# Kernel optimization log

Hardware: AMD Instinct MI355X
Metric: run time of the kernel (lower is better)

The kernel has to match this reference:

```python
import jax, jax.numpy as jnp
import numpy as np

B, t, FEAT, N, E = 128, 16, 256, 1024, 8192


def setup_inputs() -> dict:
    key = jax.random.key(0)
    k = jax.random.split(key, 9)
    s = 1.0 / np.sqrt(FEAT).astype(np.float32)
    x = jax.random.normal(k[0], (B, t, FEAT), jnp.float32)
    nodes = jax.random.normal(k[1], (B, N, FEAT), jnp.float32)
    edges = jax.random.randint(k[2], (B, 2, E), 0, 256).astype(jnp.int32)
    weights = jax.random.uniform(k[3], (B, 1, E), jnp.float32)
    T = jax.random.randint(k[4], (B,), 0, N - t).astype(jnp.int32)
    taus = jnp.full((B,), t, dtype=jnp.int32)  # no ragged padding: taus == t
    W_self1 = jax.random.normal(k[5], (FEAT, FEAT), jnp.float32) * s
    W_msg1 = jax.random.normal(k[6], (FEAT, FEAT), jnp.float32) * s
    W_self2 = jax.random.normal(k[7], (FEAT, FEAT), jnp.float32) * s
    W_msg2 = jax.random.normal(k[8], (FEAT, FEAT), jnp.float32) * s
    return dict(x=x, taus=taus, nodes=nodes, edges=edges, weights=weights, T=T,
                W_self1=W_self1, W_msg1=W_msg1, W_self2=W_self2, W_msg2=W_msg2)


def _gcm(x, nodes, weights, edges, T, Ws1, Wm1, Ws2, Wm2):
    Bn, tn, feat = x.shape
    Nn = nodes.shape[1]
    # --- scatter new nodes into the fixed-size node buffer ---
    b_idx = jnp.repeat(jnp.arange(Bn), tn)                       # [B*t]
    tau_idx = (T[:, None] + jnp.arange(tn)).reshape(-1)          # [B*t]
    nodes = nodes.at[b_idx, tau_idx].set(x.reshape(Bn * tn, feat))
    # --- to_batch: flatten ragged per-batch graphs into one big graph ---
    flat = nodes.reshape(Bn * Nn, feat)                          # [B*N, feat]
    off = (jnp.arange(Bn) * Nn)[:, None]                         # per-batch node offset
    valid = (edges[:, 0] >= 0) & (edges[:, 1] >= 0)              # -1 marks invalid edges
    src = jnp.where(valid, edges[:, 0] + off, 0).reshape(-1)     # [B*E]
    dst = jnp.where(valid, edges[:, 1] + off, 0).reshape(-1)
    ew = (weights[:, 0] * valid).reshape(-1)                     # invalid edges -> weight 0
    # --- 2-layer edge-weighted GraphConv GNN (tanh activation) ---
    def layer(h, Ws, Wm):
        agg = jax.ops.segment_sum(ew[:, None] * h[src], dst, num_segments=Bn * Nn)
        return jnp.tanh(h @ Ws + agg @ Wm)
    h = layer(flat, Ws1, Wm1)
    h = layer(h, Ws2, Wm2)
    # --- gather GNN outputs for the newly inserted nodes ---
    out_idx = b_idx * Nn + tau_idx
    mx = h[out_idx].reshape(Bn, tn, feat)
    return mx, nodes


def reference(x, taus, nodes, edges, weights, T, W_self1, W_msg1, W_self2, W_msg2):
    mx, new_nodes = _gcm(x, nodes, weights, edges, T, W_self1, W_msg1, W_self2, W_msg2)
    return (mx, new_nodes, edges, weights, T + taus)
```

## Files before the change

### kernel.cpp

```cpp
#include <hip/hip_runtime.h>
#include <math.h>

#define BB    128
#define TTW   16
#define FEATN 256
#define NNODE 1024
#define NEDGE 8192
#define MROW  272
#define M1    (BB*MROW)
#define M2    (BB*TTW)

#define OUT_MX    0
#define OUT_NODES (BB*TTW*FEATN)
#define OUT_EDGES (OUT_NODES + BB*NNODE*FEATN)
#define OUT_W     (OUT_EDGES + BB*2*NEDGE)
#define OUT_TT    (OUT_W + BB*NEDGE)

typedef short bf16x8 __attribute__((ext_vector_type(8)));
typedef float f32x4  __attribute__((ext_vector_type(4)));

__device__ inline unsigned short f2bf(float f) {
    unsigned int u = __float_as_uint(f);
    return (unsigned short)((u + 0x7fffu + ((u >> 16) & 1u)) >> 16);
}
__device__ inline float tanh_fast(float x) {
    return 1.f - 2.f / (__expf(2.f * x) + 1.f);
}

__global__ void k_pass(const float4* __restrict__ nodes4, const float4* __restrict__ x4,
                       const int* __restrict__ T, float4* __restrict__ out4) {
    int idx = blockIdx.x * 256 + threadIdx.x;
    int b   = idx >> 16;
    int row = (idx >> 6) & 1023;
    int f   = idx & 63;
    int dT  = row - T[b];
    const float4* src = ((unsigned)dT < 16u) ? (x4 + ((size_t)b * 16 + dT) * 64 + f)
                                             : (nodes4 + idx);
    out4[idx] = *src;
}

__global__ void k_misc(const int4* __restrict__ e4, const float4* __restrict__ w4,
                       const int* __restrict__ T, const int* __restrict__ taus,
                       float* __restrict__ out) {
    int i = blockIdx.x * 256 + threadIdx.x;
    if (i < 524288) {
        int4 e = e4[i];
        float4 o = make_float4((float)e.x, (float)e.y, (float)e.z, (float)e.w);
        ((float4*)(out + OUT_EDGES))[i] = o;
    } else if (i < 786432) {
        ((float4*)(out + OUT_W))[i - 524288] = w4[i - 524288];
    } else if (i < 786560) {
        int b = i - 786432;
        out[OUT_TT + b] = (float)(T[b] + taus[b]);
    }
}

__global__ void k_wconv(const float* __restrict__ Ws1, const float* __restrict__ Wm1,
                        const float* __restrict__ Ws2, const float* __restrict__ Wm2,
                        unsigned short* __restrict__ Wt1, unsigned short* __restrict__ Wt2) {
    int i = blockIdx.x * 256 + threadIdx.x;
    int layer = i >> 17;
    int j = i & 131071;
    int k = j >> 8, n = j & 255;
    const float* Ws = layer ? Ws2 : Ws1;
    const float* Wm = layer ? Wm2 : Wm1;
    float v = (k < 256) ? Ws[(size_t)k * 256 + n] : Wm[(size_t)(k - 256) * 256 + n];
    unsigned short* Wt = layer ? Wt2 : Wt1;
    Wt[(size_t)n * 512 + k] = f2bf(v);
}

__global__ void k_prep_x(const float* __restrict__ nodes, const float* __restrict__ x,
                         const int* __restrict__ T, unsigned short* __restrict__ Xc1) {
    int idx = blockIdx.x * 256 + threadIdx.x;
    int g  = idx >> 5;
    int c8 = idx & 31;
    int b = g / MROW, r = g % MROW;
    int Tb = T[b];
    const float* src;
    if (r >= 256)                       src = x + ((size_t)b * 16 + (r - 256)) * 256;
    else if ((unsigned)(r - Tb) < 16u)  src = x + ((size_t)b * 16 + (r - Tb)) * 256;
    else                                src = nodes + ((size_t)b * 1024 + r) * 256;
    float4 v0 = *(const float4*)(src + c8 * 8);
    float4 v1 = *(const float4*)(src + c8 * 8 + 4);
    uint4 p;
    p.x = f2bf(v0.x) | ((unsigned)f2bf(v0.y) << 16);
    p.y = f2bf(v0.z) | ((unsigned)f2bf(v0.w) << 16);
    p.z = f2bf(v1.x) | ((unsigned)f2bf(v1.y) << 16);
    p.w = f2bf(v1.z) | ((unsigned)f2bf(v1.w) << 16);
    *(uint4*)(Xc1 + (size_t)g * 512 + c8 * 8) = p;
}

__global__ void k_bucket(const int* __restrict__ edges, const float* __restrict__ w,
                         int2* __restrict__ sw, int* __restrict__ bstart) {
    int b = blockIdx.x, tid = threadIdx.x;
    __shared__ int cnt[256];
    __shared__ int pos[256];
    cnt[tid] = 0;
    __syncthreads();
    const int* src = edges + (size_t)b * 2 * NEDGE;
    const int* dst = src + NEDGE;
    for (int e = tid; e < NEDGE; e += 256) atomicAdd(&cnt[dst[e]], 1);
    __syncthreads();
    int my = cnt[tid], v = my;
    for (int off = 1; off < 256; off <<= 1) {
        int u = 0;
        if (tid >= off) u = cnt[tid - off];
        __syncthreads();
        cnt[tid] = v = v + u;
        __syncthreads();
    }
    int start = v - my;
    bstart[b * 264 + tid] = start;
    if (tid == 0) bstart[b * 264 + 256] = NEDGE;
    pos[tid] = start;
    __syncthreads();
    const float* wb = w + (size_t)b * NEDGE;
    for (int e = tid; e < NEDGE; e += 256) {
        int d = dst[e];
        int p = atomicAdd(&pos[d], 1);
        sw[(size_t)b * NEDGE + p] = make_int2(src[e], __float_as_int(wb[e]));
    }
}

__global__ void k_agg1(const int2* __restrict__ sw, const int* __restrict__ bstart,
                       const int* __restrict__ T, unsigned short* __restrict__ Xc1) {
    int wid  = blockIdx.x * 4 + (threadIdx.x >> 6);
    int lane = threadIdx.x & 63;
    int b = wid / MROW, r = wid % MROW;
    int d = (r < 256) ? r : (T[b] + (r - 256));
    float4 acc = make_float4(0.f, 0.f, 0.f, 0.f);
    if (d < 256) {
        int e0 = bstart[b * 264 + d];
        int e1 = bstart[b * 264 + d + 1];
        const int2* swb = sw + (size_t)b * NEDGE;
        const unsigned short* Xb = Xc1 + (size_t)b * MROW * 512;
        for (int e = e0; e < e1; ++e) {
            int2 p = swb[e];
            float wt = __int_as_float(p.y);
            uint2 q = *((const uint2*)(Xb + (size_t)p.x * 512) + lane);
            acc.x = fmaf(wt, __uint_as_float(q.x << 16),          acc.x);
            acc.y = fmaf(wt, __uint_as_float(q.x & 0xffff0000u),  acc.y);
            acc.z = fmaf(wt, __uint_as_float(q.y << 16),          acc.z);
            acc.w = fmaf(wt, __uint_as_float(q.y & 0xffff0000u),  acc.w);
        }
    }
    uint2 o;
    o.x = f2bf(acc.x) | ((unsigned)f2bf(acc.y) << 16);
    o.y = f2bf(acc.z) | ((unsigned)f2bf(acc.w) << 16);
    *(uint2*)(Xc1 + (size_t)wid * 512 + 256 + lane * 4) = o;
}

template <int OBF16>
__global__ __launch_bounds__(256, 2) void k_gemm(const unsigned short* __restrict__ Xc,
                                                 const unsigned short* __restrict__ Wt,
                                                 void* __restrict__ outp) {
    int tile_m = blockIdx.x >> 1;
    int tile_n = blockIdx.x & 1;
    int tid  = threadIdx.x;
    int wv   = tid >> 6, lane = tid & 63;
    int wm   = wv >> 1, wn = wv & 1;
    int lm   = lane & 15, lq = lane >> 4;

    __shared__ short As[128 * 32];
    __shared__ short Bs[128 * 32];

    f32x4 acc[4][4];
#pragma unroll
    for (int mi = 0; mi < 4; ++mi)
#pragma unroll
        for (int ni = 0; ni < 4; ++ni) acc[mi][ni] = (f32x4){0.f, 0.f, 0.f, 0.f};

    for (int kc = 0; kc < 16; ++kc) {
        if (kc) __syncthreads();
#pragma unroll
        for (int p = 0; p < 2; ++p) {
            int slot = p * 256 + tid;
            int row = slot >> 2, seg = slot & 3;
            ((uint4*)As)[slot] = *(const uint4*)(Xc + ((size_t)(tile_m * 128 + row)) * 512 + kc * 32 + seg * 8);
            ((uint4*)Bs)[slot] = *(const uint4*)(Wt + ((size_t)(tile_n * 128 + row)) * 512 + kc * 32 + seg * 8);
        }
        __syncthreads();

        bf16x8 af[4], bfr[4];
#pragma unroll
        for (int mi = 0; mi < 4; ++mi)
            af[mi] = ((const bf16x8*)As)[(wm * 64 + mi * 16 + lm) * 4 + lq];
#pragma unroll
        for (int ni = 0; ni < 4; ++ni)
            bfr[ni] = ((const bf16x8*)Bs)[(wn * 64 + ni * 16 + lm) * 4 + lq];
#pragma unroll
        for (int mi = 0; mi < 4; ++mi)
#pragma unroll
            for (int ni = 0; ni < 4; ++ni)
                acc[mi][ni] = __builtin_amdgcn_mfma_f32_16x16x32_bf16(af[mi], bfr[ni], acc[mi][ni], 0, 0, 0);
    }

#pragma unroll
    for (int mi = 0; mi < 4; ++mi) {
#pragma unroll
        for (int ni = 0; ni < 4; ++ni) {
            int n = tile_n * 128 + wn * 64 + ni * 16 + lm;
#pragma unroll
            for (int r = 0; r < 4; ++r) {
                int m = tile_m * 128 + wm * 64 + mi * 16 + lq * 4 + r;
                float v = tanh_fast(acc[mi][ni][r]);
                if (OBF16) ((unsigned short*)outp)[(size_t)m * 256 + n] = f2bf(v);
                else       ((float*)outp)[(size_t)m * 256 + n] = v;
            }
        }
    }
}

__global__ void k_agg2(const unsigned short* __restrict__ h1, const int2* __restrict__ sw,
                       const int* __restrict__ bstart, const int* __restrict__ T,
                       unsigned short* __restrict__ Xc2) {
    int g2   = blockIdx.x * 4 + (threadIdx.x >> 6);
    int lane = threadIdx.x & 63;
    int b = g2 >> 4, i = g2 & 15;
    ((uint2*)(Xc2 + (size_t)g2 * 512))[lane] =
        ((const uint2*)(h1 + (size_t)(b * MROW + 256 + i) * 256))[lane];
    int d = T[b] + i;
    float4 acc = make_float4(0.f, 0.f, 0.f, 0.f);
    if (d < 256) {
        int e0 = bstart[b * 264 + d];
        int e1 = bstart[b * 264 + d + 1];
        const int2* swb = sw + (size_t)b * NEDGE;
        const unsigned short* hb = h1 + (size_t)b * MROW * 256;
        for (int e = e0; e < e1; ++e) {
            int2 p = swb[e];
            float wt = __int_as_float(p.y);
            uint2 q = *((const uint2*)(hb + (size_t)p.x * 256) + lane);
            acc.x = fmaf(wt, __uint_as_float(q.x << 16),          acc.x);
            acc.y = fmaf(wt, __uint_as_float(q.x & 0xffff0000u),  acc.y);
            acc.z = fmaf(wt, __uint_as_float(q.y << 16),          acc.z);
            acc.w = fmaf(wt, __uint_as_float(q.y & 0xffff0000u),  acc.w);
        }
    }
    uint2 o;
    o.x = f2bf(acc.x) | ((unsigned)f2bf(acc.y) << 16);
    o.y = f2bf(acc.z) | ((unsigned)f2bf(acc.w) << 16);
    *(uint2*)(Xc2 + (size_t)g2 * 512 + 256 + lane * 4) = o;
}

extern "C" void kernel_launch(void* const* d_in, const int* in_sizes, int n_in,
                              void* d_out, int out_size, void* d_ws, size_t ws_size,
                              hipStream_t stream) {
    const float* x       = (const float*)d_in[0];
    const int*   taus    = (const int*)d_in[1];
    const float* nodes   = (const float*)d_in[2];
    const int*   edges   = (const int*)d_in[3];
    const float* weights = (const float*)d_in[4];
    const int*   T       = (const int*)d_in[5];
    const float* Ws1     = (const float*)d_in[6];
    const float* Wm1     = (const float*)d_in[7];
    const float* Ws2     = (const float*)d_in[8];
    const float* Wm2     = (const float*)d_in[9];
    float* out = (float*)d_out;

    char* ws = (char*)d_ws;
    int2*           sw     = (int2*)ws;
    int*            bstart = (int*)(ws + 8388608);
    unsigned short* Xc1    = (unsigned short*)(ws + 8523776);
    unsigned short* h1     = (unsigned short*)(ws + 44175360);
    unsigned short* Xc2    = (unsigned short*)(ws + 62001152);
    unsigned short* Wt1    = (unsigned short*)(ws + 64098304);
    unsigned short* Wt2    = (unsigned short*)(ws + 64360448);

    float* out_nodes = out + OUT_NODES;

    k_pass  <<<32768, 256, 0, stream>>>((const float4*)nodes, (const float4*)x, T, (float4*)out_nodes);
    k_misc  <<<3073, 256, 0, stream>>>((const int4*)edges, (const float4*)weights, T, taus, out);
    k_wconv <<<1024, 256, 0, stream>>>(Ws1, Wm1, Ws2, Wm2, Wt1, Wt2);
    k_prep_x<<<4352, 256, 0, stream>>>(nodes, x, T, Xc1);
    k_bucket<<<BB, 256, 0, stream>>>(edges, weights, sw, bstart);
    k_agg1  <<<8704, 256, 0, stream>>>(sw, bstart, T, Xc1);
    k_gemm<1><<<272 * 2, 256, 0, stream>>>(Xc1, Wt1, h1);
    k_agg2  <<<512, 256, 0, stream>>>(h1, sw, bstart, T, Xc2);
    k_gemm<0><<<16 * 2, 256, 0, stream>>>(Xc2, Wt2, out + OUT_MX);
}
```

Measured before the change: 470.0 us.

## Replace layer-1 sparse gather aggregation with dense adjacency MFMA GEMM

Builds a dense per-batch 256x256 fp32 weighted adjacency matrix using atomic adds, transposes the bf16 node features, and computes the layer-1 aggregation as a batched bf16 MFMA GEMM instead of a per-destination edge gather loop. A small kernel then copies the aggregation rows for the inserted window. This trades irregular gathers for dense matrix work. It adds zeroing and atomic scatter over a 32 MB adjacency buffer, a transpose kernel, and rounds the edge weights to bf16, which can lose precision.

```diff
diff --git a/kernel.cpp b/kernel.cpp
--- a/kernel.cpp
+++ b/kernel.cpp
@@ -8,7 +8,6 @@
 #define NEDGE 8192
 #define MROW  272
 #define M1    (BB*MROW)
-#define M2    (BB*TTW)
 
 #define OUT_MX    0
 #define OUT_NODES (BB*TTW*FEATN)
@@ -90,6 +89,44 @@
     *(uint4*)(Xc1 + (size_t)g * 512 + c8 * 8) = p;
 }
 
+__global__ void k_xt(const unsigned short* __restrict__ Xc1, unsigned short* __restrict__ Xt) {
+    int b  = blockIdx.x >> 4;
+    int tr = (blockIdx.x >> 2) & 3;
+    int tc = blockIdx.x & 3;
+    __shared__ unsigned short S[64][72];
+#pragma unroll
+    for (int p = 0; p < 2; ++p) {
+        int slot = p * 256 + threadIdx.x;
+        int r = slot >> 3, c8 = slot & 7;
+        uint4 v = *(const uint4*)(Xc1 + ((size_t)(b * MROW + tr * 64 + r)) * 512 + tc * 64 + c8 * 8);
+        *(uint4*)&S[r][c8 * 8] = v;
+    }
+    __syncthreads();
+#pragma unroll
+    for (int p = 0; p < 2; ++p) {
+        int slot = p * 256 + threadIdx.x;
+        int r2 = slot >> 3, c8 = slot & 7;
+        unsigned short tmp[8];
+#pragma unroll
+        for (int j = 0; j < 8; ++j) tmp[j] = S[c8 * 8 + j][r2];
+        *(uint4*)(Xt + ((size_t)b << 16) + (size_t)(tc * 64 + r2) * 256 + tr * 64 + c8 * 8) = *(uint4*)tmp;
+    }
+}
+
+__global__ void k_zero(float4* __restrict__ p) {
+    int i = blockIdx.x * 256 + threadIdx.x;
+    p[i] = make_float4(0.f, 0.f, 0.f, 0.f);
+}
+
+__global__ void k_adj(const int* __restrict__ edges, const float* __restrict__ w,
+                      float* __restrict__ W_adj) {
+    int i = blockIdx.x * 256 + threadIdx.x;
+    int b = i >> 13, e = i & 8191;
+    const int* eb = edges + (size_t)b * 2 * NEDGE;
+    int s = eb[e], d = eb[NEDGE + e];
+    atomicAdd(&W_adj[((size_t)b << 16) + (d << 8) + s], w[(size_t)b * NEDGE + e]);
+}
+
 __global__ void k_bucket(const int* __restrict__ edges, const float* __restrict__ w,
                          int2* __restrict__ sw, int* __restrict__ bstart) {
     int b = blockIdx.x, tid = threadIdx.x;
@@ -122,32 +159,88 @@
     }
 }
 
-__global__ void k_agg1(const int2* __restrict__ sw, const int* __restrict__ bstart,
-                       const int* __restrict__ T, unsigned short* __restrict__ Xc1) {
-    int wid  = blockIdx.x * 4 + (threadIdx.x >> 6);
-    int lane = threadIdx.x & 63;
-    int b = wid / MROW, r = wid % MROW;
-    int d = (r < 256) ? r : (T[b] + (r - 256));
-    float4 acc = make_float4(0.f, 0.f, 0.f, 0.f);
-    if (d < 256) {
-        int e0 = bstart[b * 264 + d];
-        int e1 = bstart[b * 264 + d + 1];
-        const int2* swb = sw + (size_t)b * NEDGE;
-        const unsigned short* Xb = Xc1 + (size_t)b * MROW * 512;
-        for (int e = e0; e < e1; ++e) {
-            int2 p = swb[e];
-            float wt = __int_as_float(p.y);
-            uint2 q = *((const uint2*)(Xb + (size_t)p.x * 512) + lane);
-            acc.x = fmaf(wt, __uint_as_float(q.x << 16),          acc.x);
-            acc.y = fmaf(wt, __uint_as_float(q.x & 0xffff0000u),  acc.y);
-            acc.z = fmaf(wt, __uint_as_float(q.y << 16),          acc.z);
-            acc.w = fmaf(wt, __uint_as_float(q.y & 0xffff0000u),  acc.w);
-        }
-    }
-    uint2 o;
-    o.x = f2bf(acc.x) | ((unsigned)f2bf(acc.y) << 16);
-    o.y = f2bf(acc.z) | ((unsigned)f2bf(acc.w) << 16);
-    *(uint2*)(Xc1 + (size_t)wid * 512 + 256 + lane * 4) = o;
+__global__ __launch_bounds__(256, 2) void k_aggemm(const float* __restrict__ W_adj,
+                                                   const unsigned short* __restrict__ Xt,
+                                                   unsigned short* __restrict__ Xc1) {
+    int b = blockIdx.x >> 2;
+    int tile_m = (blockIdx.x >> 1) & 1, tile_n = blockIdx.x & 1;
+    int tid = threadIdx.x;
+    int wv = tid >> 6, lane = tid & 63;
+    int wm = wv >> 1, wn = wv & 1;
+    int lm = lane & 15, lq = lane >> 4;
+
+    __shared__ short As[128 * 32];
+    __shared__ short Bs[128 * 32];
+
+    f32x4 acc[4][4];
+#pragma unroll
+    for (int mi = 0; mi < 4; ++mi)
+#pragma unroll
+        for (int ni = 0; ni < 4; ++ni) acc[mi][ni] = (f32x4){0.f, 0.f, 0.f, 0.f};
+
+    const float* Ab = W_adj + ((size_t)b << 16) + (size_t)tile_m * 128 * 256;
+    const unsigned short* Bb = Xt + ((size_t)b << 16) + (size_t)tile_n * 128 * 256;
+
+    for (int kc = 0; kc < 8; ++kc) {
+        if (kc) __syncthreads();
+#pragma unroll
+        for (int p = 0; p < 4; ++p) {
+            int slot = p * 256 + tid;
+            int row = slot >> 3, seg = slot & 7;
+            float4 v = *(const float4*)(Ab + (size_t)row * 256 + kc * 32 + seg * 4);
+            uint2 pk;
+            pk.x = f2bf(v.x) | ((unsigned)f2bf(v.y) << 16);
+            pk.y = f2bf(v.z) | ((unsigned)f2bf(v.w) << 16);
+            *(uint2*)(As + row * 32 + seg * 4) = pk;
+        }
+#pragma unroll
+        for (int p = 0; p < 2; ++p) {
+            int slot = p * 256 + tid;
+            int row = slot >> 2, seg = slot & 3;
+            ((uint4*)Bs)[slot] = *(const uint4*)(Bb + (size_t)row * 256 + kc * 32 + seg * 8);
+        }
+        __syncthreads();
+
+        bf16x8 af[4], bfr[4];
+#pragma unroll
+        for (int mi = 0; mi < 4; ++mi)
+            af[mi] = ((const bf16x8*)As)[(wm * 64 + mi * 16 + lm) * 4 + lq];
+#pragma unroll
+        for (int ni = 0; ni < 4; ++ni)
+            bfr[ni] = ((const bf16x8*)Bs)[(wn * 64 + ni * 16 + lm) * 4 + lq];
+#pragma unroll
+        for (int mi = 0; mi < 4; ++mi)
+#pragma unroll
+            for (int ni = 0; ni < 4; ++ni)
+                acc[mi][ni] = __builtin_amdgcn_mfma_f32_16x16x32_bf16(af[mi], bfr[ni], acc[mi][ni], 0, 0, 0);
+    }
+
+#pragma unroll
+    for (int mi = 0; mi < 4; ++mi) {
+#pragma unroll
+        for (int ni = 0; ni < 4; ++ni) {
+            int n = tile_n * 128 + wn * 64 + ni * 16 + lm;
+#pragma unroll
+            for (int r = 0; r < 4; ++r) {
+                int m = tile_m * 128 + wm * 64 + mi * 16 + lq * 4 + r;
+                Xc1[((size_t)(b * MROW + m)) * 512 + 256 + n] = f2bf(acc[mi][ni][r]);
+            }
+        }
+    }
+}
+
+__global__ void k_fixwin(const int* __restrict__ T, unsigned short* __restrict__ Xc1) {
+    int b = blockIdx.x;
+    int Tb = T[b];
+#pragma unroll
+    for (int p = 0; p < 2; ++p) {
+        int slot = p * 256 + threadIdx.x;
+        int i = slot >> 5, c = slot & 31;
+        int d = Tb + i;
+        uint4 v = make_uint4(0u, 0u, 0u, 0u);
+        if (d < 256) v = *(const uint4*)(Xc1 + ((size_t)(b * MROW + d)) * 512 + 256 + c * 8);
+        *(uint4*)(Xc1 + ((size_t)(b * MROW + 256 + i)) * 512 + 256 + c * 8) = v;
+    }
 }
 
 template <int OBF16>
@@ -262,19 +355,25 @@
     int*            bstart = (int*)(ws + 8388608);
     unsigned short* Xc1    = (unsigned short*)(ws + 8523776);
     unsigned short* h1     = (unsigned short*)(ws + 44175360);
+    unsigned short* Xt     = (unsigned short*)(ws + 44175360);
     unsigned short* Xc2    = (unsigned short*)(ws + 62001152);
     unsigned short* Wt1    = (unsigned short*)(ws + 64098304);
     unsigned short* Wt2    = (unsigned short*)(ws + 64360448);
+    float*          W_adj  = (float*)(ws + 64622592);
 
     float* out_nodes = out + OUT_NODES;
 
-    k_pass  <<<32768, 256, 0, stream>>>((const float4*)nodes, (const float4*)x, T, (float4*)out_nodes);
-    k_misc  <<<3073, 256, 0, stream>>>((const int4*)edges, (const float4*)weights, T, taus, out);
-    k_wconv <<<1024, 256, 0, stream>>>(Ws1, Wm1, Ws2, Wm2, Wt1, Wt2);
-    k_prep_x<<<4352, 256, 0, stream>>>(nodes, x, T, Xc1);
-    k_bucket<<<BB, 256, 0, stream>>>(edges, weights, sw, bstart);
-    k_agg1  <<<8704, 256, 0, stream>>>(sw, bstart, T, Xc1);
+    k_pass   <<<32768, 256, 0, stream>>>((const float4*)nodes, (const float4*)x, T, (float4*)out_nodes);
+    k_misc   <<<3073, 256, 0, stream>>>((const int4*)edges, (const float4*)weights, T, taus, out);
+    k_wconv  <<<1024, 256, 0, stream>>>(Ws1, Wm1, Ws2, Wm2, Wt1, Wt2);
+    k_prep_x <<<4352, 256, 0, stream>>>(nodes, x, T, Xc1);
+    k_xt     <<<2048, 256, 0, stream>>>(Xc1, Xt);
+    k_zero   <<<8192, 256, 0, stream>>>((float4*)W_adj);
+    k_adj    <<<4096, 256, 0, stream>>>(edges, weights, W_adj);
+    k_bucket <<<BB, 256, 0, stream>>>(edges, weights, sw, bstart);
+    k_aggemm <<<512, 256, 0, stream>>>(W_adj, Xt, Xc1);
+    k_fixwin <<<BB, 256, 0, stream>>>(T, Xc1);
     k_gemm<1><<<272 * 2, 256, 0, stream>>>(Xc1, Wt1, h1);
-    k_agg2  <<<512, 256, 0, stream>>>(h1, sw, bstart, T, Xc2);
+    k_agg2   <<<512, 256, 0, stream>>>(h1, sw, bstart, T, Xc2);
     k_gemm<0><<<16 * 2, 256, 0, stream>>>(Xc2, Wt2, out + OUT_MX);
 }
```

After: 463.9 us. Within noise of the previous version (-1.3%).
